# Performance work log

Measured on AMD Instinct MI355X. Metric: run time of the kernel, lower is better.

Reference implementation:

```python
import jax, jax.numpy as jnp
import numpy as np

N_NODES = 100000
N_EDGES = 1600000
IN_F = 64
OUT_F = 32
NEG_SLOPE = 0.2


def setup_inputs() -> dict:
    key = jax.random.key(0)
    k = jax.random.split(key, 6)
    x = jax.random.normal(k[0], (N_NODES, IN_F), dtype=jnp.float32)
    edge_index = jax.random.randint(k[1], (2, N_EDGES), 0, N_NODES, dtype=jnp.int64)
    W = jax.random.normal(k[2], (IN_F, OUT_F), dtype=jnp.float32) * 0.1
    att_src = jax.random.normal(k[3], (OUT_F,), dtype=jnp.float32) * 0.1
    att_dst = jax.random.normal(k[4], (OUT_F,), dtype=jnp.float32) * 0.1
    bias = jax.random.normal(k[5], (OUT_F,), dtype=jnp.float32) * 0.1
    return {"x": x, "edge_index": edge_index, "W": W,
            "att_src": att_src, "att_dst": att_dst, "bias": bias}


def reference(x, edge_index, W, att_src, att_dst, bias):
    N = x.shape[0]
    # Linear projection (single head, concat=True -> [N, OUT_F])
    h = x @ W  # [N, C]
    a_src = h @ att_src  # [N] per-node source attention logit contribution
    a_dst = h @ att_dst  # [N] per-node destination contribution
    # add self loops (PyG GATConv default add_self_loops=True)
    loop = jnp.arange(N, dtype=edge_index.dtype)
    src = jnp.concatenate([edge_index[0], loop])  # [E+N] message senders
    dst = jnp.concatenate([edge_index[1], loop])  # [E+N] message receivers
    # attention logits per edge, LeakyReLU(alpha_src[j] + alpha_dst[i])
    e = jax.nn.leaky_relu(a_src[src] + a_dst[dst], NEG_SLOPE)
    # segment softmax over incoming edges of each destination node
    m = jax.ops.segment_max(e, dst, num_segments=N)  # every node has a self loop
    ex = jnp.exp(e - m[dst])
    denom = jax.ops.segment_sum(ex, dst, num_segments=N)
    alpha = ex / denom[dst]  # [E+N]
    # weighted scatter-add of source features into destinations
    out = jax.ops.segment_sum(h[src] * alpha[:, None], dst, num_segments=N)
    out = out + bias
    # GATLayer activation='relu'
    return jax.nn.relu(out)
```

## Files before the change

kernel.cpp:

```cpp
#include <hip/hip_runtime.h>
#include <hip/hip_fp16.h>
#include <math.h>

#define IN_F 64
#define OUT_F 32
#define NEG_SLOPE 0.2f

#define BK_SHIFT 6
#define BK 64
#define NBMAX 2048
#define NBLKA 256
#define PSTAGE 3
#define CAPSHIFT 11
#define CAP 2048
#define COLCAP 2048

typedef _Float16 half8_t __attribute__((ext_vector_type(8)));
typedef float float4_t __attribute__((ext_vector_type(4)));
typedef int int4_t __attribute__((ext_vector_type(4)));


__device__ __forceinline__ float leaky(float v) {
    return (v > 0.0f) ? v : NEG_SLOPE * v;
}

__device__ __forceinline__ int incScan512(int v, int tid, int* wsum) {
    const int lane = tid & 63, wid = tid >> 6;
    #pragma unroll
    for (int m = 1; m < 64; m <<= 1) {
        int u = __shfl_up(v, m);
        if (lane >= m) v += u;
    }
    if (lane == 63) wsum[wid] = v;
    __syncthreads();
    int add = 0;
    for (int k = 0; k < wid; ++k) add += wsum[k];
    __syncthreads();
    return v + add;
}

__global__ __launch_bounds__(256) void k_proj(
        const float* __restrict__ x, const float* __restrict__ W,
        const float* __restrict__ att_src, const float* __restrict__ att_dst,
        __half2* __restrict__ h2, float* __restrict__ asrc, float* __restrict__ adst,
        int* __restrict__ cursor, int N, int NB, int PB) {
    const int tid = threadIdx.x;

    if (blockIdx.x >= PB) {
        for (int b = tid; b < NB; b += 256) cursor[b] = b << CAPSHIFT;
        if (tid < 16) h2[(size_t)N * 16 + tid] = __floats2half2_rn(0.0f, 0.0f);
        if (tid == 16) asrc[N] = -1e30f;
        return;
    }

    const int wv   = tid >> 6;
    const int lane = tid & 63;
    const int m    = lane & 15;
    const int quad = lane >> 4;
    const int node0 = (blockIdx.x * 4 + wv) * 16;
    if (node0 >= N) return;

    const int kb = quad * 8;
    half8_t b00, b01, b10, b11;
    #pragma unroll
    for (int j = 0; j < 8; ++j) {
        b00[j] = (_Float16)W[(kb + j) * OUT_F + m];
        b01[j] = (_Float16)W[(32 + kb + j) * OUT_F + m];
        b10[j] = (_Float16)W[(kb + j) * OUT_F + 16 + m];
        b11[j] = (_Float16)W[(32 + kb + j) * OUT_F + 16 + m];
    }
    const int row = min(node0 + m, N - 1);
    const float* xr = x + (size_t)row * IN_F + kb;
    float4_t xa = *(const float4_t*)(xr);
    float4_t xb = *(const float4_t*)(xr + 4);
    float4_t xc = *(const float4_t*)(xr + 32);
    float4_t xd = *(const float4_t*)(xr + 36);
    half8_t a0, a1;
    #pragma unroll
    for (int j = 0; j < 4; ++j) {
        a0[j] = (_Float16)xa[j]; a0[4 + j] = (_Float16)xb[j];
        a1[j] = (_Float16)xc[j]; a1[4 + j] = (_Float16)xd[j];
    }
    float4_t acc0 = {0.f, 0.f, 0.f, 0.f};
    float4_t acc1 = {0.f, 0.f, 0.f, 0.f};
    acc0 = __builtin_amdgcn_mfma_f32_16x16x32_f16(a0, b00, acc0, 0, 0, 0);
    acc0 = __builtin_amdgcn_mfma_f32_16x16x32_f16(a1, b01, acc0, 0, 0, 0);
    acc1 = __builtin_amdgcn_mfma_f32_16x16x32_f16(a0, b10, acc1, 0, 0, 0);
    acc1 = __builtin_amdgcn_mfma_f32_16x16x32_f16(a1, b11, acc1, 0, 0, 0);

    const float aS0 = att_src[m], aS1 = att_src[16 + m];
    const float aD0 = att_dst[m], aD1 = att_dst[16 + m];
    #pragma unroll
    for (int r = 0; r < 4; ++r) {
        const int node = node0 + quad * 4 + r;
        float h0 = acc0[r], h1 = acc1[r];
        float h0p = __shfl_xor(h0, 1);
        float h1p = __shfl_xor(h1, 1);
        if (node < N && (m & 1) == 0) {
            __half2 hv;
            hv.x = __float2half_rn(h0); hv.y = __float2half_rn(h0p);
            h2[(size_t)node * 16 + (m >> 1)] = hv;
            __half2 hw;
            hw.x = __float2half_rn(h1); hw.y = __float2half_rn(h1p);
            h2[(size_t)node * 16 + 8 + (m >> 1)] = hw;
        }
        float vs = h0 * aS0 + h1 * aS1;
        float vd = h0 * aD0 + h1 * aD1;
        #pragma unroll
        for (int mm = 1; mm < 16; mm <<= 1) {
            vs += __shfl_xor(vs, mm);
            vd += __shfl_xor(vd, mm);
        }
        if (node < N && m == 0) {
            asrc[node] = vs;
            adst[node] = vd;
        }
    }
}

__global__ __launch_bounds__(512) void k_bpart(const int* __restrict__ src,
                                               const int* __restrict__ dst,
                                               int* __restrict__ cursor,
                                               int* __restrict__ recs,
                                               int NB, int E, int epb) {
    __shared__ int cnt[NBMAX];
    __shared__ int lcur[NBMAX];
    const int tid = threadIdx.x, blk = blockIdx.x;
    for (int b = tid; b < NB; b += 512) cnt[b] = 0;
    __syncthreads();
    const int e0 = blk * epb, e1 = min(E, e0 + epb);
    for (int e = e0 + tid; e < e1; e += 512)
        atomicAdd(&cnt[dst[e] >> BK_SHIFT], 1);
    __syncthreads();
    for (int b = tid; b < NB; b += 512) {
        const int c = cnt[b];
        if (c > 0) lcur[b] = atomicAdd(&cursor[b], c);
    }
    __syncthreads();
    for (int e = e0 + tid; e < e1; e += 512) {
        int s = src[e];
        int d = dst[e];
        int p = atomicAdd(&lcur[d >> BK_SHIFT], 1);
        recs[p] = ((d & (BK - 1)) << 17) | s;
    }
}

__global__ __launch_bounds__(512) void k_pg(const int* __restrict__ recs,
                                            const int* __restrict__ cursor,
                                            const float* __restrict__ asrc,
                                            const float* __restrict__ adst,
                                            const __half2* __restrict__ h2,
                                            const float* __restrict__ bias,
                                            float* __restrict__ out,
                                            int NB, int E, int N) {
    __shared__ __align__(16) int colsh[COLCAP];
    __shared__ int fineCnt[BK];
    __shared__ int cur[BK];
    __shared__ int loff[BK];
    __shared__ int lpad[BK];
    __shared__ int wsum[8];
    const int b = blockIdx.x, tid = threadIdx.x;
    const int node0 = b << BK_SHIFT;

    const int cb0 = b << CAPSHIFT;
    const int count = min(cursor[b] - cb0, CAP);

    for (int i = tid; i < COLCAP; i += 512) colsh[i] = N;
    if (tid < BK) fineCnt[tid] = 0;
    __syncthreads();

    int myrec[PSTAGE];
    #pragma unroll
    for (int k = 0; k < PSTAGE; ++k) {
        int i = tid + k * 512;
        if (i < count) {
            int v = recs[cb0 + i];
            myrec[k] = v;
            atomicAdd(&fineCnt[v >> 17], 1);
        }
    }
    for (int i = tid + PSTAGE * 512; i < count; i += 512)
        atomicAdd(&fineCnt[recs[cb0 + i] >> 17], 1);
    __syncthreads();

    const int v0 = (tid < BK) ? fineCnt[tid] : 0;
    const int pv = (v0 + 3) & ~3;
    const int vin = (tid < BK) ? pv : 0;
    const int pinc = incScan512(vin, tid, wsum);
    const int pexcl = pinc - vin;
    if (tid < BK) {
        loff[tid] = pexcl;
        lpad[tid] = pv;
        cur[tid]  = pexcl;
    }
    __syncthreads();

    #pragma unroll
    for (int k = 0; k < PSTAGE; ++k) {
        int i = tid + k * 512;
        if (i < count) {
            int r = myrec[k];
            int p = atomicAdd(&cur[r >> 17], 1);
            colsh[p] = r & 0x1FFFF;
        }
    }
    for (int i = tid + PSTAGE * 512; i < count; i += 512) {
        int r = recs[cb0 + i];
        int p = atomicAdd(&cur[r >> 17], 1);
        colsh[p] = r & 0x1FFFF;
    }
    __syncthreads();

    const int wid  = tid >> 6;
    const int lane = tid & 63;
    const int g    = lane >> 4;
    const int c2   = lane & 15;
    for (int i = 0; i < 8; ++i) {
        const int dloc = wid * 8 + i;
        const int n = node0 + dloc;
        if (n >= N) break;
        const float adst_n = adst[n];
        float l = 0.0f, accx = 0.0f, accy = 0.0f;
        if (g == 0) {
            float p = __expf(leaky(asrc[n] + adst_n));
            float2 hv = __half22float2(h2[(size_t)n * 16 + c2]);
            l = p; accx = p * hv.x; accy = p * hv.y;
        }
        const int base = loff[dloc];
        const int nch  = lpad[dloc] >> 2;
        for (int c = g; c < nch; c += 4) {
            const int4_t cc = *(const int4_t*)(&colsh[base + c * 4]);
            const int s0 = cc[0], s1 = cc[1], s2 = cc[2], s3 = cc[3];
            float a0 = asrc[s0], a1 = asrc[s1], a2 = asrc[s2], a3 = asrc[s3];
            float2 h0 = __half22float2(h2[(size_t)s0 * 16 + c2]);
            float2 h1 = __half22float2(h2[(size_t)s1 * 16 + c2]);
            float2 hv2 = __half22float2(h2[(size_t)s2 * 16 + c2]);
            float2 h3 = __half22float2(h2[(size_t)s3 * 16 + c2]);
            float p0 = __expf(leaky(a0 + adst_n));
            float p1 = __expf(leaky(a1 + adst_n));
            float p2 = __expf(leaky(a2 + adst_n));
            float p3 = __expf(leaky(a3 + adst_n));
            l += (p0 + p1) + (p2 + p3);
            accx += p0 * h0.x + p1 * h1.x + p2 * hv2.x + p3 * h3.x;
            accy += p0 * h0.y + p1 * h1.y + p2 * hv2.y + p3 * h3.y;
        }
        l    += __shfl_xor(l, 16);    l    += __shfl_xor(l, 32);
        accx += __shfl_xor(accx, 16); accx += __shfl_xor(accx, 32);
        accy += __shfl_xor(accy, 16); accy += __shfl_xor(accy, 32);
        if (g == 0) {
            float inv = 1.0f / l;
            float2 bb = ((const float2*)bias)[c2];
            float2 o;
            o.x = fmaxf(accx * inv + bb.x, 0.0f);
            o.y = fmaxf(accy * inv + bb.y, 0.0f);
            ((float2*)out)[(size_t)n * 16 + c2] = o;
        }
    }
}

extern "C" void kernel_launch(void* const* d_in, const int* in_sizes, int n_in,
                              void* d_out, int out_size, void* d_ws, size_t ws_size,
                              hipStream_t stream) {
    const float* x        = (const float*)d_in[0];
    const int*   eidx     = (const int*)d_in[1];
    const float* W        = (const float*)d_in[2];
    const float* att_src  = (const float*)d_in[3];
    const float* att_dst  = (const float*)d_in[4];
    const float* bias     = (const float*)d_in[5];
    float* out = (float*)d_out;

    const int N = in_sizes[0] / IN_F;
    const int E = in_sizes[1] / 2;
    const int* src = eidx;
    const int* dst = eidx + E;

    const int NB  = (N + BK - 1) >> BK_SHIFT;
    const int epb = (E + NBLKA - 1) / NBLKA;

    int* u = (int*)d_ws;
    size_t o = 0;
    __half2* h2     = (__half2*)(u + o); o += (size_t)(N + 1) * 16;
    float*   asrc   = (float*)(u + o);   o += N + 1;
    float*   adst   = (float*)(u + o);   o += N;
    int*     cursor = u + o;             o += NBMAX;
    int*     recs   = u + o;             o += (size_t)NBMAX * CAP;

    const int PB = (N + 63) / 64;

    k_proj<<<PB + 1, 256, 0, stream>>>(x, W, att_src, att_dst, h2, asrc, adst,
                                       cursor, N, NB, PB);
    k_bpart<<<NBLKA, 512, 0, stream>>>(src, dst, cursor, recs, NB, E, epb);
    k_pg<<<NB, 512, 0, stream>>>(recs, cursor, asrc, adst, h2, bias, out, NB, E, N);
}
```

Before: 153.6 us.

## Fuse edge bucketing into projection kernel using per-edge global atomics

Drops the separate bucket-partition kernel and folds edge bucketing into the projection launch as 2048 extra blocks. Each edge now reserves its slot with a global atomicAdd on its bucket cursor. Previously, block-level LDS histograms first aggregated counts and then claimed bucket ranges. Cursors are zeroed with a memset, and buckets now start at offset zero relative to a fixed base. This removes one kernel launch and lets bucketing overlap with the projection work, at the cost of many contended global atomics in place of locally aggregated ones.

```diff
diff --git a/kernel.cpp b/kernel.cpp
--- a/kernel.cpp
+++ b/kernel.cpp
@@ -9,7 +9,7 @@
 #define BK_SHIFT 6
 #define BK 64
 #define NBMAX 2048
-#define NBLKA 256
+#define NPART 2048
 #define PSTAGE 3
 #define CAPSHIFT 11
 #define CAP 2048
@@ -39,17 +39,30 @@
     return v + add;
 }
 
-__global__ __launch_bounds__(256) void k_proj(
+__global__ __launch_bounds__(256) void k_projpart(
         const float* __restrict__ x, const float* __restrict__ W,
         const float* __restrict__ att_src, const float* __restrict__ att_dst,
         __half2* __restrict__ h2, float* __restrict__ asrc, float* __restrict__ adst,
-        int* __restrict__ cursor, int N, int NB, int PB) {
+        const int* __restrict__ src, const int* __restrict__ dst,
+        int* __restrict__ cursor, int* __restrict__ recs,
+        int N, int E, int PB) {
     const int tid = threadIdx.x;
 
-    if (blockIdx.x >= PB) {
-        for (int b = tid; b < NB; b += 256) cursor[b] = b << CAPSHIFT;
+    if (blockIdx.x >= PB + NPART) {
         if (tid < 16) h2[(size_t)N * 16 + tid] = __floats2half2_rn(0.0f, 0.0f);
         if (tid == 16) asrc[N] = -1e30f;
+        return;
+    }
+    if (blockIdx.x >= PB) {
+        const int blk = blockIdx.x - PB;
+        for (int e = blk * 256 + tid; e < E; e += NPART * 256) {
+            const int s = src[e];
+            const int d = dst[e];
+            const int b = d >> BK_SHIFT;
+            const int idx = atomicAdd(&cursor[b], 1);
+            if (idx < CAP)
+                recs[((size_t)b << CAPSHIFT) + idx] = ((d & (BK - 1)) << 17) | s;
+        }
         return;
     }
 
@@ -115,33 +128,6 @@
             asrc[node] = vs;
             adst[node] = vd;
         }
-    }
-}
-
-__global__ __launch_bounds__(512) void k_bpart(const int* __restrict__ src,
-                                               const int* __restrict__ dst,
-                                               int* __restrict__ cursor,
-                                               int* __restrict__ recs,
-                                               int NB, int E, int epb) {
-    __shared__ int cnt[NBMAX];
-    __shared__ int lcur[NBMAX];
-    const int tid = threadIdx.x, blk = blockIdx.x;
-    for (int b = tid; b < NB; b += 512) cnt[b] = 0;
-    __syncthreads();
-    const int e0 = blk * epb, e1 = min(E, e0 + epb);
-    for (int e = e0 + tid; e < e1; e += 512)
-        atomicAdd(&cnt[dst[e] >> BK_SHIFT], 1);
-    __syncthreads();
-    for (int b = tid; b < NB; b += 512) {
-        const int c = cnt[b];
-        if (c > 0) lcur[b] = atomicAdd(&cursor[b], c);
-    }
-    __syncthreads();
-    for (int e = e0 + tid; e < e1; e += 512) {
-        int s = src[e];
-        int d = dst[e];
-        int p = atomicAdd(&lcur[d >> BK_SHIFT], 1);
-        recs[p] = ((d & (BK - 1)) << 17) | s;
     }
 }
 
@@ -162,8 +148,8 @@
     const int b = blockIdx.x, tid = threadIdx.x;
     const int node0 = b << BK_SHIFT;
 
-    const int cb0 = b << CAPSHIFT;
-    const int count = min(cursor[b] - cb0, CAP);
+    const size_t cb0 = (size_t)b << CAPSHIFT;
+    const int count = min(cursor[b], CAP);
 
     for (int i = tid; i < COLCAP; i += 512) colsh[i] = N;
     if (tid < BK) fineCnt[tid] = 0;
@@ -275,7 +261,6 @@
     const int* dst = eidx + E;
 
     const int NB  = (N + BK - 1) >> BK_SHIFT;
-    const int epb = (E + NBLKA - 1) / NBLKA;
 
     int* u = (int*)d_ws;
     size_t o = 0;
@@ -287,8 +272,9 @@
 
     const int PB = (N + 63) / 64;
 
-    k_proj<<<PB + 1, 256, 0, stream>>>(x, W, att_src, att_dst, h2, asrc, adst,
-                                       cursor, N, NB, PB);
-    k_bpart<<<NBLKA, 512, 0, stream>>>(src, dst, cursor, recs, NB, E, epb);
+    hipMemsetAsync(cursor, 0, NBMAX * sizeof(int), stream);
+    k_projpart<<<PB + NPART + 1, 256, 0, stream>>>(x, W, att_src, att_dst,
+                                                   h2, asrc, adst, src, dst,
+                                                   cursor, recs, N, E, PB);
     k_pg<<<NB, 512, 0, stream>>>(recs, cursor, asrc, adst, h2, bias, out, NB, E, N);
 }
```

After: 369.1 us. +140.4%, slower.
